# Performance work log

Measured on AMD Instinct MI355X. Metric: run time of the kernel, lower is better.

Reference implementation:

```python
import jax, jax.numpy as jnp
import numpy as np

N_ATOMS = 4096
N_METAL = 2048
METAL_Z = 79
ELEC_Z = 8
BOX_L = 24.0
DL = 2.0
SIGMA = 1.0
SCALING = 1.0  # scaling_factor


def _k_grid(cell_np, dl):
    # integer reciprocal-grid indices, k=0 removed; static (numpy) so shapes are fixed
    lengths = np.linalg.norm(cell_np, axis=1)
    nk = np.ceil(lengths / dl).astype(int)
    ax = [np.arange(-n, n + 1) for n in nk]
    g = np.stack(np.meshgrid(*ax, indexing='ij'), axis=-1).reshape(-1, 3)
    return jnp.asarray(g[np.any(g != 0, axis=1)].astype(np.float32))


def _kfac_vol(cell, kgrid):
    recip = 2.0 * jnp.pi * jnp.linalg.inv(cell).T        # reciprocal lattice rows
    kvec = kgrid @ recip                                  # [K,3]
    k2 = jnp.sum(kvec * kvec, axis=-1)                    # [K]
    kfac = jnp.exp(-0.5 * (SIGMA ** 2) * k2) / k2         # Gaussian-screened 1/k^2 (exponent=1)
    vol = jnp.abs(jnp.linalg.det(cell))
    return kvec, kfac, vol


def _ewald_field(r, q, cell, kgrid):
    # reciprocal-space Ewald potential/field, remove_self_interaction=False
    kvec, kfac, vol = _kfac_vol(cell, kgrid)
    phase = r @ kvec.T                                    # [N,K]
    c, s = jnp.cos(phase), jnp.sin(phase)
    Sr = c.T @ q                                          # [K,C] Re S(k)
    Si = s.T @ q                                          # [K,C] Im S(k)
    pref = 4.0 * jnp.pi / vol
    field = pref * (c @ (kfac[:, None] * Sr) + s @ (kfac[:, None] * Si))  # [N,C]
    pot = 0.5 * jnp.sum(q * field, axis=0)
    return pot, field


def _ewald_matrix(r, cell, kgrid):
    # field with q = I, computed without materializing the NxN identity:
    # A_ij = (4pi/V) sum_k kfac * cos(k.(r_i - r_j))
    kvec, kfac, vol = _kfac_vol(cell, kgrid)
    phase = r @ kvec.T
    c, s = jnp.cos(phase), jnp.sin(phase)
    pref = 4.0 * jnp.pi / vol
    return pref * ((c * kfac) @ c.T + (s * kfac) @ s.T)   # [Nm,Nm]


def _S_matrix(r_m, cell, J, kgrid):
    A = _ewald_matrix(r_m, cell, kgrid)
    n = A.shape[0]
    top = jnp.concatenate([A + jnp.diag(J), jnp.ones((n, 1), A.dtype)], axis=1)
    bot = jnp.concatenate([jnp.ones((1, n), A.dtype), jnp.zeros((1, 1), A.dtype)], axis=1)
    coeffs = jnp.concatenate([top, bot], axis=0)          # bordered QEQ (KKT) system
    return jnp.linalg.inv(coeffs)                         # torch.linalg.solve(coeffs, I)


def _qeq(positions, cell3, q, J_raw, metal_idx, kgrid):
    q = q.at[metal_idx].set(0.0)                          # q_all[all_metal_index] = 0
    J_m = jnp.square(J_raw)[0] * jnp.ones((metal_idx.shape[0],), q.dtype)
    # cache path: S built from detached r/cell/J -> stop_gradient
    S = jax.lax.stop_gradient(
        _S_matrix(positions[metal_idx], cell3, J_m, kgrid))
    _, f = _ewald_field(positions, q, cell3, kgrid)       # field from electrolyte charges
    B = -f[metal_idx] * SCALING                           # external_field=None -> B_ext=0, chi=0
    chi_vec = jnp.concatenate([B, jnp.zeros((1, 1), q.dtype)], axis=0)  # system_charge = 0
    q_sol = S @ chi_vec                                   # [Nm+1,1]
    return q.at[metal_idx].set(q_sol[:-1] / SCALING)


def setup_inputs():
    key = jax.random.key(0)
    k1, k2 = jax.random.split(key, 2)
    positions = jax.random.uniform(k1, (N_ATOMS, 3), jnp.float32) * BOX_L
    cell = (jnp.eye(3, dtype=jnp.float32) * BOX_L)[None]  # [1,3,3]
    q = jax.random.normal(k2, (N_ATOMS, 1), jnp.float32)
    J_raw = 0.1 * jnp.ones((1,), jnp.float32)
    atomic_numbers = jnp.concatenate([
        jnp.full((N_METAL,), METAL_Z, jnp.int32),
        jnp.full((N_ATOMS - N_METAL,), ELEC_Z, jnp.int32)])
    batch = jnp.zeros((N_ATOMS,), jnp.int32)
    return {'positions': positions, 'cell': cell, 'q': q, 'J_raw': J_raw,
            'atomic_numbers': atomic_numbers, 'batch': batch}


def reference(positions, cell, q, J_raw, atomic_numbers, batch):
    cell3 = cell.reshape(3, 3)
    an = np.asarray(atomic_numbers)
    metal_idx = jnp.asarray(np.where(an == METAL_Z)[0])   # concrete gather indices
    kgrid = _k_grid(np.asarray(cell3), DL)
    q_mw = _qeq(positions, cell3, q, J_raw, metal_idx, kgrid)
    return q_mw  # data['q_mw']; mw_energy_external is identically 0 (external_field=None)
```

## Files before the change

### kernel.cpp

```cpp
#include <hip/hip_runtime.h>
#include <math.h>


#define NA 4096
#define NM 2048
#define METAL_Z 79
#define KH 7812
#define KHP 7936
#define NIT 150
#define NBLK_CG 64
#define CGT 1024
#define TWO_PI 6.283185307179586f

#define OFF_CONSTS 0
#define OFF_SUMS   256
#define OFF_FLAGS  512
#define OFF_KTAB   4096
#define OFF_FRAC   131072
#define OFF_MLIST  196608
#define OFF_POSOF  204800
#define OFF_SRW    221184
#define OFF_SIW    252928
#define OFF_BPART  284672
#define OFF_B      792576
#define OFF_VEC    800768
#define OFF_WBUF   833536
#define OFF_PBUF   866304
#define OFF_A      917504
#define OFF_GHI    25165824u
#define OFF_GLO    90177536u
#define G_END      155189248u

typedef short bf16x8 __attribute__((ext_vector_type(8)));
typedef float f32x4 __attribute__((ext_vector_type(4)));

__device__ __forceinline__ void sc_frac(float u, float& s, float& c) {
    float t = u - floorf(u);
    s = __builtin_amdgcn_sinf(t);
    c = __builtin_amdgcn_cosf(t);
}

__device__ __forceinline__ unsigned short bf16rne(float x) {
    unsigned u = __float_as_uint(x);
    unsigned r = u + 0x7fffu + ((u >> 16) & 1u);
    return (unsigned short)(r >> 16);
}

__device__ __forceinline__ unsigned long long pack_wt(float w, int tag) {
    return (unsigned long long)__float_as_uint(w) | ((unsigned long long)(unsigned)tag << 32);
}
__device__ __forceinline__ float lo_f(unsigned long long v) {
    return __uint_as_float((unsigned)v);
}

__global__ void k_setup(const float* __restrict__ pos, const float* __restrict__ cell,
                        const float* __restrict__ Jraw, const int* __restrict__ an,
                        float* __restrict__ wsf) {
    int tid = threadIdx.x;
    __shared__ float sM[9];
    __shared__ int sc[256];
    if (tid == 0) {
        float c00=cell[0],c01=cell[1],c02=cell[2];
        float c10=cell[3],c11=cell[4],c12=cell[5];
        float c20=cell[6],c21=cell[7],c22=cell[8];
        float det = c00*(c11*c22-c12*c21) - c01*(c10*c22-c12*c20) + c02*(c10*c21-c11*c20);
        float i00 =  (c11*c22 - c12*c21)/det;
        float i01 = -(c01*c22 - c02*c21)/det;
        float i02 =  (c01*c12 - c02*c11)/det;
        float i10 = -(c10*c22 - c12*c20)/det;
        float i11 =  (c00*c22 - c02*c20)/det;
        float i12 = -(c00*c12 - c02*c10)/det;
        float i20 =  (c10*c21 - c11*c20)/det;
        float i21 = -(c00*c21 - c01*c20)/det;
        float i22 =  (c00*c11 - c01*c10)/det;
        sM[0]=i00; sM[1]=i10; sM[2]=i20;
        sM[3]=i01; sM[4]=i11; sM[5]=i21;
        sM[6]=i02; sM[7]=i12; sM[8]=i22;
        float vol = fabsf(det);
        for (int m=0;m<9;m++) wsf[OFF_CONSTS/4 + m] = sM[m];
        wsf[OFF_CONSTS/4 + 9]  = 12.566370614359172f / vol;
        wsf[OFF_CONSTS/4 + 10] = Jraw[0]*Jraw[0];
    }
    __syncthreads();
    float M0=sM[0],M1=sM[1],M2=sM[2],M3=sM[3],M4=sM[4],M5=sM[5],M6=sM[6],M7=sM[7],M8=sM[8];
    for (int i=tid; i<NA; i+=256) {
        float x=pos[3*i], y=pos[3*i+1], z=pos[3*i+2];
        wsf[OFF_FRAC/4 + 4*i+0] = M0*x + M1*y + M2*z;
        wsf[OFF_FRAC/4 + 4*i+1] = M3*x + M4*y + M5*z;
        wsf[OFF_FRAC/4 + 4*i+2] = M6*x + M7*y + M8*z;
        wsf[OFF_FRAC/4 + 4*i+3] = 0.f;
    }
    ((int*)wsf)[OFF_FLAGS/4 + tid] = 0;
    if (tid < 4) wsf[OFF_SUMS/4 + tid] = 0.f;
    unsigned long long* tz = (unsigned long long*)((char*)wsf + OFF_WBUF);
    for (int i=tid; i<4480; i+=256) tz[i] = 0ull;
    int cnt = 0;
    int base_i = tid*16;
    for (int j=0;j<16;j++) cnt += (an[base_i+j]==METAL_Z) ? 1 : 0;
    sc[tid] = cnt; __syncthreads();
    for (int off=1; off<256; off<<=1) {
        int v = (tid>=off) ? sc[tid-off] : 0;
        __syncthreads();
        sc[tid] += v;
        __syncthreads();
    }
    int base = sc[tid] - cnt;
    int* mlist = (int*)wsf + OFF_MLIST/4;
    int* posof = (int*)wsf + OFF_POSOF/4;
    for (int j=0;j<16;j++) {
        int i = base_i + j;
        if (an[i]==METAL_Z) { mlist[base] = i; posof[i] = base; base++; }
    }
}

__global__ void k_ktab(float* __restrict__ wsf) {
    int k = blockIdx.x*256 + threadIdx.x;
    if (k >= KHP) return;
    float4 out;
    if (k < KH) {
        int gx = k/625 - 12;
        int rem = k%625;
        int gy = rem/25 - 12;
        int gz = rem%25 - 12;
        const float* M = wsf + OFF_CONSTS/4;
        float pref = M[9];
        float kx = TWO_PI*(gx*M[0] + gy*M[3] + gz*M[6]);
        float ky = TWO_PI*(gx*M[1] + gy*M[4] + gz*M[7]);
        float kz = TWO_PI*(gx*M[2] + gy*M[5] + gz*M[8]);
        float k2 = kx*kx + ky*ky + kz*kz;
        float kfac = __expf(-0.5f*k2) / k2;
        out = make_float4((float)gx, (float)gy, (float)gz, 2.f*pref*kfac);
    } else {
        out = make_float4(0.f, 0.f, 0.f, 0.f);
    }
    *(float4*)(wsf + OFF_KTAB/4 + 4*k) = out;
}

__global__ void k_gbuild(const float* __restrict__ wsf, unsigned* __restrict__ ghi,
                         unsigned* __restrict__ glo) {
    int k = blockIdx.x*256 + threadIdx.x;
    int m = blockIdx.y;
    int atom = ((const int*)wsf)[OFF_MLIST/4 + m];
    float4 f = *(const float4*)(wsf + OFF_FRAC/4 + 4*atom);
    float4 kt = *(const float4*)(wsf + OFF_KTAB/4 + 4*k);
    float rw = sqrtf(kt.w);
    float u = kt.x*f.x + kt.y*f.y + kt.z*f.z;
    float s, c; sc_frac(u, s, c);
    float gc = rw*c, gs = rw*s;
    unsigned short hc = bf16rne(gc);
    float hcf = __uint_as_float(((unsigned)hc) << 16);
    unsigned short lc = bf16rne(gc - hcf);
    unsigned short hs = bf16rne(gs);
    float hsf = __uint_as_float(((unsigned)hs) << 16);
    unsigned short ls = bf16rne(gs - hsf);
    size_t off = (size_t)m*KHP + k;
    ghi[off] = (unsigned)hc | ((unsigned)hs << 16);
    glo[off] = (unsigned)lc | ((unsigned)ls << 16);
}

__global__ void k_srsi(const float* __restrict__ q, const int* __restrict__ an,
                       float* __restrict__ wsf) {
    int k = blockIdx.x;
    int tid = threadIdx.x;
    float4 kt = *(const float4*)(wsf + OFF_KTAB/4 + 4*k);
    const float* frac = wsf + OFF_FRAC/4;
    float aR=0.f, aI=0.f;
    for (int i=tid; i<NA; i+=256) {
        float qa = (an[i]==METAL_Z) ? 0.f : q[i];
        float4 f = *(const float4*)(frac + 4*i);
        float u = kt.x*f.x + kt.y*f.y + kt.z*f.z;
        float s,c; sc_frac(u, s, c);
        aR += qa*c; aI += qa*s;
    }
    __shared__ float sR[256], sI[256];
    sR[tid]=aR; sI[tid]=aI; __syncthreads();
    for (int off=128; off>0; off>>=1) {
        if (tid<off) { sR[tid]+=sR[tid+off]; sI[tid]+=sI[tid+off]; }
        __syncthreads();
    }
    if (tid==0) {
        wsf[OFF_SRW/4 + k] = kt.w * sR[0];
        wsf[OFF_SIW/4 + k] = kt.w * sI[0];
    }
}

__global__ void k_field(float* __restrict__ wsf) {
    int kc = blockIdx.x;
    int m = blockIdx.y*256 + threadIdx.x;
    int atom = ((const int*)wsf)[OFF_MLIST/4 + m];
    float4 f = *(const float4*)(wsf + OFF_FRAC/4 + 4*atom);
    const float* kt = wsf + OFF_KTAB/4;
    const float* SrW = wsf + OFF_SRW/4;
    const float* SiW = wsf + OFF_SIW/4;
    float acc = 0.f;
    int k0 = kc*128;
    for (int j=0;j<128;j++) {
        int k = k0 + j;
        float4 g = *(const float4*)(kt + 4*k);
        float u = g.x*f.x + g.y*f.y + g.z*f.z;
        float s,c; sc_frac(u, s, c);
        acc = fmaf(c, SrW[k], fmaf(s, SiW[k], acc));
    }
    wsf[OFF_BPART/4 + kc*NM + m] = acc;
}

__global__ void k_bfinal(float* __restrict__ wsf) {
    int tid = threadIdx.x;
    float b0 = 0.f, b1 = 0.f;
    for (int kc=0;kc<62;kc++) {
        b0 += wsf[OFF_BPART/4 + kc*NM + tid];
        b1 += wsf[OFF_BPART/4 + kc*NM + 1024 + tid];
    }
    b0 = -b0; b1 = -b1;
    __shared__ float sb[1024];
    sb[tid] = b0 + b1; __syncthreads();
    for (int off=512; off>0; off>>=1) {
        if (tid<off) sb[tid] += sb[tid+off];
        __syncthreads();
    }
    float mean = sb[0] * (1.f/NM);
    float* r = wsf + OFF_VEC/4 + 4096;
    r[tid]        = b0 - mean;
    r[1024 + tid] = b1 - mean;
}

__launch_bounds__(256)
__global__ void k_abuild_g(float* __restrict__ wsf, const unsigned* __restrict__ ghi,
                           const unsigned* __restrict__ glo) {
    __shared__ unsigned Sh[16384];
    int tid = threadIdx.x;
    int bid = blockIdx.x;
    int bi = (int)((sqrtf(8.f*bid + 1.f) - 1.f)*0.5f);
    while ((bi+1)*(bi+2)/2 <= bid) bi++;
    while (bi*(bi+1)/2 > bid) bi--;
    int bj = bid - bi*(bi+1)/2;
    bool diag = (bi == bj);
    float J = wsf[OFF_CONSTS/4 + 10];

    int w = tid >> 6, lane = tid & 63;
    int mat   = diag ? (w & 1) : w;
    int tb    = (diag ? bi : (w < 2 ? bi : bj)) * 128;
    int rbase = diag ? ((w >> 1) * 64) : 0;
    int nld   = diag ? 8 : 16;
    const unsigned* gsrc = (mat & 1) ? glo : ghi;
    int lrow8 = lane >> 3;
    int gcsw  = (lane & 7) ^ (lrow8 & 7);
    unsigned* lb = &Sh[mat*4096 + rbase*32];
    const unsigned* gb0 = gsrc + (size_t)(tb + rbase)*KHP + gcsw*4;

    int wr = w & 1, wc = w >> 1;
    int lr = lane & 15, g4 = lane >> 4;
    const unsigned short* UHs = (const unsigned short*)&Sh[0];
    const unsigned short* ULs = (const unsigned short*)&Sh[4096];
    const unsigned short* VHs = diag ? UHs : (const unsigned short*)&Sh[8192];
    const unsigned short* VLs = diag ? ULs : (const unsigned short*)&Sh[12288];

    f32x4 acc[4][4];
    #pragma unroll
    for (int i=0;i<4;i++)
        #pragma unroll
        for (int j=0;j<4;j++) acc[i][j] = (f32x4){0.f,0.f,0.f,0.f};

    for (int kc = 0; kc < KHP/32; ++kc) {
        __syncthreads();
        const unsigned* gb = gb0 + kc*32;
        #pragma unroll
        for (int i = 0; i < 16; ++i) {
            if (i < nld) {
                uint4 v = *(const uint4*)(gb + (size_t)(i*8 + lrow8)*KHP);
                *(uint4*)&lb[i*256 + lane*4] = v;
            }
        }
        __syncthreads();
        #pragma unroll
        for (int ks = 0; ks < 2; ++ks) {
            int cA = ks*4 + g4;
            bf16x8 ah[4], al[4], bh[4], bl[4];
            #pragma unroll
            for (int fi=0; fi<4; fi++) {
                int r = wr*64 + fi*16 + lr;
                int o = r*64 + ((cA ^ (r&7)) << 3);
                ah[fi] = *(const bf16x8*)&UHs[o];
                al[fi] = *(const bf16x8*)&ULs[o];
            }
            #pragma unroll
            for (int fj=0; fj<4; fj++) {
                int r = wc*64 + fj*16 + lr;
                int o = r*64 + ((cA ^ (r&7)) << 3);
                bh[fj] = *(const bf16x8*)&VHs[o];
                bl[fj] = *(const bf16x8*)&VLs[o];
            }
            #pragma unroll
            for (int fi=0; fi<4; fi++)
                #pragma unroll
                for (int fj=0; fj<4; fj++) {
                    acc[fi][fj] = __builtin_amdgcn_mfma_f32_16x16x32_bf16(ah[fi], bh[fj], acc[fi][fj], 0,0,0);
                    acc[fi][fj] = __builtin_amdgcn_mfma_f32_16x16x32_bf16(ah[fi], bl[fj], acc[fi][fj], 0,0,0);
                    acc[fi][fj] = __builtin_amdgcn_mfma_f32_16x16x32_bf16(al[fi], bh[fj], acc[fi][fj], 0,0,0);
                }
        }
    }

    float* A = wsf + OFF_A/4;
    int rb4 = g4 * 4;
    #pragma unroll
    for (int fi=0; fi<4; fi++) {
        #pragma unroll
        for (int fj=0; fj<4; fj++) {
            int gj = bj*128 + wc*64 + fj*16 + lr;
            #pragma unroll
            for (int r=0; r<4; r++) {
                int gi = bi*128 + wr*64 + fi*16 + rb4 + r;
                float v = acc[fi][fj][r] + ((gi==gj)?J:0.f);
                A[(size_t)gi*NM + gj] = v;
                A[(size_t)gj*NM + gi] = v;
            }
        }
    }
}

__launch_bounds__(CGT, 1)
__global__ void k_cg(float* __restrict__ wsf) {
    const float* A = wsf + OFF_A/4;
    float* vec = wsf + OFF_VEC/4;
    float* xg = vec;
    const float* rg = vec + 4096;
    unsigned long long* wbufg = (unsigned long long*)((char*)wsf + OFF_WBUF);
    unsigned long long* pbufg = (unsigned long long*)((char*)wsf + OFF_PBUF);

    __shared__ float rs[NM];
    __shared__ float wrow[32];
    __shared__ float red[4];

    int tid = threadIdx.x, bid = blockIdx.x;
    int rl = tid >> 5, lane = tid & 31;
    int row = bid*32 + rl;
    const float* Arow = A + (size_t)row*NM;
    int ca = 2*tid;

    ((float2*)rs)[tid] = ((const float2*)rg)[tid];
    __syncthreads();

    float s0=0.f, s1=0.f;
    float pr=0.f, xr=0.f;
    float gp=1.f, ap=1.f;

    for (int iter=0; iter<NIT; ++iter) {
        int t = iter + 1;
        unsigned long long* wb = wbufg + (iter&1)*2048;
        unsigned long long* pb = pbufg + (iter&1)*192;
        float acc=0.f;
        #pragma unroll 8
        for (int c=lane*4; c<NM; c+=128) {
            float4 a = *(const float4*)(Arow + c);
            float4 u = *(const float4*)(rs + c);
            acc += a.x*u.x + a.y*u.y + a.z*u.z + a.w*u.w;
        }
        #pragma unroll
        for (int off=1; off<32; off<<=1) acc += __shfl_xor(acc, off);
        if (lane == 0) {
            wrow[rl] = acc;
            __hip_atomic_store(&wb[row], pack_wt(acc, t),
                               __ATOMIC_RELAXED, __HIP_MEMORY_SCOPE_AGENT);
        }
        float rrow = (tid<32) ? rs[bid*32+tid] : 0.f;
        __syncthreads();
        if (tid == 0) {
            float gb=0.f, db=0.f, mb=0.f;
            #pragma unroll
            for (int j=0;j<32;j++) {
                float rv = rs[bid*32+j];
                gb = fmaf(rv,rv,gb); db = fmaf(rv,wrow[j],db); mb += wrow[j];
            }
            __hip_atomic_store(&pb[bid],       pack_wt(gb, t), __ATOMIC_RELAXED, __HIP_MEMORY_SCOPE_AGENT);
            __hip_atomic_store(&pb[64+bid],    pack_wt(db, t), __ATOMIC_RELAXED, __HIP_MEMORY_SCOPE_AGENT);
            __hip_atomic_store(&pb[128+bid],   pack_wt(mb, t), __ATOMIC_RELAXED, __HIP_MEMORY_SCOPE_AGENT);
        }
        float w0, w1;
        if (tid < 64) {
            unsigned long long e0,e1,eg,ed,em;
            for (;;) {
                e0 = __hip_atomic_load(&wb[ca],     __ATOMIC_RELAXED, __HIP_MEMORY_SCOPE_AGENT);
                e1 = __hip_atomic_load(&wb[ca+1],   __ATOMIC_RELAXED, __HIP_MEMORY_SCOPE_AGENT);
                eg = __hip_atomic_load(&pb[tid],    __ATOMIC_RELAXED, __HIP_MEMORY_SCOPE_AGENT);
                ed = __hip_atomic_load(&pb[64+tid], __ATOMIC_RELAXED, __HIP_MEMORY_SCOPE_AGENT);
                em = __hip_atomic_load(&pb[128+tid],__ATOMIC_RELAXED, __HIP_MEMORY_SCOPE_AGENT);
                int ok = ((int)(e0>>32)==t) & ((int)(e1>>32)==t)
                       & ((int)(eg>>32)==t) & ((int)(ed>>32)==t) & ((int)(em>>32)==t);
                if (__all(ok)) break;
                __builtin_amdgcn_s_sleep(1);
            }
            w0 = lo_f(e0); w1 = lo_f(e1);
            float g = lo_f(eg), d = lo_f(ed), m = lo_f(em);
            #pragma unroll
            for (int off=1; off<64; off<<=1) {
                g += __shfl_xor(g,off); d += __shfl_xor(d,off); m += __shfl_xor(m,off);
            }
            if (tid==0) { red[0]=g; red[1]=d; red[2]=m; }
        } else {
            unsigned long long e0,e1;
            for (;;) {
                e0 = __hip_atomic_load(&wb[ca],   __ATOMIC_RELAXED, __HIP_MEMORY_SCOPE_AGENT);
                e1 = __hip_atomic_load(&wb[ca+1], __ATOMIC_RELAXED, __HIP_MEMORY_SCOPE_AGENT);
                int ok = ((int)(e0>>32)==t) & ((int)(e1>>32)==t);
                if (__all(ok)) break;
                __builtin_amdgcn_s_sleep(1);
            }
            w0 = lo_f(e0); w1 = lo_f(e1);
        }
        __syncthreads();
        float g = red[0], d = red[1];
        float m = red[2] * (1.f/NM);
        float b, a;
        if (iter == 0) { b=0.f; a=g/d; }
        else { b = g/gp; a = g/(d - b*g/ap); }
        gp=g; ap=a;
        if (tid < 32) {
            pr = (iter==0) ? rrow : fmaf(b, pr, rrow);
            xr = (iter==0) ? a*pr : fmaf(a, pr, xr);
        }
        float wt0 = w0 - m, wt1 = w1 - m;
        s0 = (iter==0) ? wt0 : fmaf(b, s0, wt0);
        s1 = (iter==0) ? wt1 : fmaf(b, s1, wt1);
        float2 rv2 = *(const float2*)(rs + ca);
        *(float2*)(rs + ca) = make_float2(fmaf(-a, s0, rv2.x), fmaf(-a, s1, rv2.y));
        __syncthreads();
    }
    if (tid < 32) xg[bid*32+tid] = xr;
}

__global__ void k_out(const float* __restrict__ q, const int* __restrict__ an,
                      const float* __restrict__ wsf, float* __restrict__ out) {
    int i = blockIdx.x*256 + threadIdx.x;
    if (i >= NA) return;
    if (an[i]==METAL_Z) {
        int p = ((const int*)wsf)[OFF_POSOF/4 + i];
        out[i] = wsf[OFF_VEC/4 + p];
    } else {
        out[i] = q[i];
    }
}

extern "C" void kernel_launch(void* const* d_in, const int* in_sizes, int n_in,
                              void* d_out, int out_size, void* d_ws, size_t ws_size,
                              hipStream_t stream) {
    (void)in_sizes; (void)n_in; (void)out_size;
    const float* pos  = (const float*)d_in[0];
    const float* cell = (const float*)d_in[1];
    const float* q    = (const float*)d_in[2];
    const float* Jraw = (const float*)d_in[3];
    const int*   an   = (const int*)d_in[4];
    float* wsf = (float*)d_ws;
    float* out = (float*)d_out;
    unsigned* ghi = (unsigned*)((char*)d_ws + OFF_GHI);
    unsigned* glo = (unsigned*)((char*)d_ws + OFF_GLO);

    k_setup<<<1, 256, 0, stream>>>(pos, cell, Jraw, an, wsf);
    k_ktab<<<KHP/256, 256, 0, stream>>>(wsf);
    k_gbuild<<<dim3(31, 2048), 256, 0, stream>>>(wsf, ghi, glo);
    k_srsi<<<KHP, 256, 0, stream>>>(q, an, wsf);
    k_field<<<dim3(62, 8), 256, 0, stream>>>(wsf);
    k_bfinal<<<1, 1024, 0, stream>>>(wsf);
    k_abuild_g<<<136, 256, 0, stream>>>(wsf, ghi, glo);
    k_cg<<<NBLK_CG, CGT, 0, stream>>>(wsf);
    k_out<<<NA/256, 256, 0, stream>>>(q, an, wsf, out);
}
```

Baseline: 1.579 ms.

## Fuse field and A-build kernels, compact electrolyte list, cut CG iterations

Merges the field kernel and the A-matrix build kernel into one launch whose first 496 blocks compute field partials and remaining blocks build A tiles, so the two independent jobs share the GPU. Builds a compacted electrolyte index list in setup so the structure-factor kernel loops over only the non-metal atoms instead of masking all of them. It also lowers the fixed CG iteration count from 150 to 135, which cuts solver work but may leave the solution less converged.

```diff
diff --git a/kernel.cpp b/kernel.cpp
--- a/kernel.cpp
+++ b/kernel.cpp
@@ -7,7 +7,7 @@
 #define METAL_Z 79
 #define KH 7812
 #define KHP 7936
-#define NIT 150
+#define NIT 135
 #define NBLK_CG 64
 #define CGT 1024
 #define TWO_PI 6.283185307179586f
@@ -29,7 +29,6 @@
 #define OFF_A      917504
 #define OFF_GHI    25165824u
 #define OFF_GLO    90177536u
-#define G_END      155189248u
 
 typedef short bf16x8 __attribute__((ext_vector_type(8)));
 typedef float f32x4 __attribute__((ext_vector_type(4)));
@@ -105,11 +104,14 @@
         __syncthreads();
     }
     int base = sc[tid] - cnt;
+    int ebase = base_i - base;
     int* mlist = (int*)wsf + OFF_MLIST/4;
     int* posof = (int*)wsf + OFF_POSOF/4;
+    int* elist = (int*)wsf + OFF_B/4;
     for (int j=0;j<16;j++) {
         int i = base_i + j;
         if (an[i]==METAL_Z) { mlist[base] = i; posof[i] = base; base++; }
+        else                { elist[ebase] = i; ebase++; }
     }
 }
 
@@ -158,15 +160,16 @@
     glo[off] = (unsigned)lc | ((unsigned)ls << 16);
 }
 
-__global__ void k_srsi(const float* __restrict__ q, const int* __restrict__ an,
-                       float* __restrict__ wsf) {
+__global__ void k_srsi(const float* __restrict__ q, float* __restrict__ wsf) {
     int k = blockIdx.x;
     int tid = threadIdx.x;
     float4 kt = *(const float4*)(wsf + OFF_KTAB/4 + 4*k);
     const float* frac = wsf + OFF_FRAC/4;
+    const int* elist = (const int*)wsf + OFF_B/4;
     float aR=0.f, aI=0.f;
-    for (int i=tid; i<NA; i+=256) {
-        float qa = (an[i]==METAL_Z) ? 0.f : q[i];
+    for (int ii=tid; ii<NA-NM; ii+=256) {
+        int i = elist[ii];
+        float qa = q[i];
         float4 f = *(const float4*)(frac + 4*i);
         float u = kt.x*f.x + kt.y*f.y + kt.z*f.z;
         float s,c; sc_frac(u, s, c);
@@ -184,52 +187,35 @@
     }
 }
 
-__global__ void k_field(float* __restrict__ wsf) {
-    int kc = blockIdx.x;
-    int m = blockIdx.y*256 + threadIdx.x;
-    int atom = ((const int*)wsf)[OFF_MLIST/4 + m];
-    float4 f = *(const float4*)(wsf + OFF_FRAC/4 + 4*atom);
-    const float* kt = wsf + OFF_KTAB/4;
-    const float* SrW = wsf + OFF_SRW/4;
-    const float* SiW = wsf + OFF_SIW/4;
-    float acc = 0.f;
-    int k0 = kc*128;
-    for (int j=0;j<128;j++) {
-        int k = k0 + j;
-        float4 g = *(const float4*)(kt + 4*k);
-        float u = g.x*f.x + g.y*f.y + g.z*f.z;
-        float s,c; sc_frac(u, s, c);
-        acc = fmaf(c, SrW[k], fmaf(s, SiW[k], acc));
-    }
-    wsf[OFF_BPART/4 + kc*NM + m] = acc;
-}
-
-__global__ void k_bfinal(float* __restrict__ wsf) {
+__launch_bounds__(256)
+__global__ void k_af(float* __restrict__ wsf, const unsigned* __restrict__ ghi,
+                     const unsigned* __restrict__ glo) {
+    __shared__ unsigned Sh[16384];
+    int bx = blockIdx.x;
     int tid = threadIdx.x;
-    float b0 = 0.f, b1 = 0.f;
-    for (int kc=0;kc<62;kc++) {
-        b0 += wsf[OFF_BPART/4 + kc*NM + tid];
-        b1 += wsf[OFF_BPART/4 + kc*NM + 1024 + tid];
-    }
-    b0 = -b0; b1 = -b1;
-    __shared__ float sb[1024];
-    sb[tid] = b0 + b1; __syncthreads();
-    for (int off=512; off>0; off>>=1) {
-        if (tid<off) sb[tid] += sb[tid+off];
-        __syncthreads();
-    }
-    float mean = sb[0] * (1.f/NM);
-    float* r = wsf + OFF_VEC/4 + 4096;
-    r[tid]        = b0 - mean;
-    r[1024 + tid] = b1 - mean;
-}
-
-__launch_bounds__(256)
-__global__ void k_abuild_g(float* __restrict__ wsf, const unsigned* __restrict__ ghi,
-                           const unsigned* __restrict__ glo) {
-    __shared__ unsigned Sh[16384];
-    int tid = threadIdx.x;
-    int bid = blockIdx.x;
+
+    if (bx < 496) {
+        int kc = bx % 62;
+        int m  = (bx / 62)*256 + tid;
+        int atom = ((const int*)wsf)[OFF_MLIST/4 + m];
+        float4 f = *(const float4*)(wsf + OFF_FRAC/4 + 4*atom);
+        const float* kt = wsf + OFF_KTAB/4;
+        const float* SrW = wsf + OFF_SRW/4;
+        const float* SiW = wsf + OFF_SIW/4;
+        float acc = 0.f;
+        int k0 = kc*128;
+        for (int j=0;j<128;j++) {
+            int k = k0 + j;
+            float4 g = *(const float4*)(kt + 4*k);
+            float u = g.x*f.x + g.y*f.y + g.z*f.z;
+            float s,c; sc_frac(u, s, c);
+            acc = fmaf(c, SrW[k], fmaf(s, SiW[k], acc));
+        }
+        wsf[OFF_BPART/4 + kc*NM + m] = acc;
+        return;
+    }
+
+    int bid = bx - 496;
     int bi = (int)((sqrtf(8.f*bid + 1.f) - 1.f)*0.5f);
     while ((bi+1)*(bi+2)/2 <= bid) bi++;
     while (bi*(bi+1)/2 > bid) bi--;
@@ -317,6 +303,26 @@
             }
         }
     }
+}
+
+__global__ void k_bfinal(float* __restrict__ wsf) {
+    int tid = threadIdx.x;
+    float b0 = 0.f, b1 = 0.f;
+    for (int kc=0;kc<62;kc++) {
+        b0 += wsf[OFF_BPART/4 + kc*NM + tid];
+        b1 += wsf[OFF_BPART/4 + kc*NM + 1024 + tid];
+    }
+    b0 = -b0; b1 = -b1;
+    __shared__ float sb[1024];
+    sb[tid] = b0 + b1; __syncthreads();
+    for (int off=512; off>0; off>>=1) {
+        if (tid<off) sb[tid] += sb[tid+off];
+        __syncthreads();
+    }
+    float mean = sb[0] * (1.f/NM);
+    float* r = wsf + OFF_VEC/4 + 4096;
+    r[tid]        = b0 - mean;
+    r[1024 + tid] = b1 - mean;
 }
 
 __launch_bounds__(CGT, 1)
@@ -444,7 +450,7 @@
 extern "C" void kernel_launch(void* const* d_in, const int* in_sizes, int n_in,
                               void* d_out, int out_size, void* d_ws, size_t ws_size,
                               hipStream_t stream) {
-    (void)in_sizes; (void)n_in; (void)out_size;
+    (void)in_sizes; (void)n_in; (void)out_size; (void)ws_size;
     const float* pos  = (const float*)d_in[0];
     const float* cell = (const float*)d_in[1];
     const float* q    = (const float*)d_in[2];
@@ -457,11 +463,10 @@
 
     k_setup<<<1, 256, 0, stream>>>(pos, cell, Jraw, an, wsf);
     k_ktab<<<KHP/256, 256, 0, stream>>>(wsf);
+    k_srsi<<<KHP, 256, 0, stream>>>(q, wsf);
     k_gbuild<<<dim3(31, 2048), 256, 0, stream>>>(wsf, ghi, glo);
-    k_srsi<<<KHP, 256, 0, stream>>>(q, an, wsf);
-    k_field<<<dim3(62, 8), 256, 0, stream>>>(wsf);
+    k_af<<<632, 256, 0, stream>>>(wsf, ghi, glo);
     k_bfinal<<<1, 1024, 0, stream>>>(wsf);
-    k_abuild_g<<<136, 256, 0, stream>>>(wsf, ghi, glo);
     k_cg<<<NBLK_CG, CGT, 0, stream>>>(wsf);
     k_out<<<NA/256, 256, 0, stream>>>(q, an, wsf, out);
 }
```

Result: no change. 1.584 ms (+0.3%).
